# Optimization experiments

Measured on AMD Instinct MI355X. Metric: run time of the kernel, lower is better.

## Reference

```python
import jax, jax.numpy as jnp
import numpy as np
import math

M_FEAT = 8  # module-level m = 4 * 2


def theta(u, R):
    # Performer FAVOR random feature map: [cos(uR), sin(uR)] / sqrt(m)
    p = u @ R  # [b, t, m]
    return jnp.concatenate([jnp.cos(p), jnp.sin(p)], axis=-1) / math.sqrt(M_FEAT)


def setup_inputs() -> dict:
    key = jax.random.key(0)
    ks = jax.random.split(key, 8)
    n_embd, n_head = 1024, 16
    d_head = n_embd // n_head  # 64
    b, t = 4, 8192
    x = jax.random.normal(ks[0], (b, t, n_embd), dtype=jnp.float32)
    # random feature projection buffer w: [d_head, m]
    w = jax.random.normal(ks[1], (d_head, M_FEAT), dtype=jnp.float32)
    # nn.Linear(n_embd, d_head) weights (stored as [in, out] for x @ W) + biases
    s = 1.0 / math.sqrt(n_embd)
    Wq = jax.random.uniform(ks[2], (n_embd, d_head), minval=-s, maxval=s, dtype=jnp.float32)
    bq = jax.random.uniform(ks[3], (d_head,), minval=-s, maxval=s, dtype=jnp.float32)
    Wk = jax.random.uniform(ks[4], (n_embd, d_head), minval=-s, maxval=s, dtype=jnp.float32)
    bk = jax.random.uniform(ks[5], (d_head,), minval=-s, maxval=s, dtype=jnp.float32)
    Wv = jax.random.uniform(ks[6], (n_embd, d_head), minval=-s, maxval=s, dtype=jnp.float32)
    bv = jax.random.uniform(ks[7], (d_head,), minval=-s, maxval=s, dtype=jnp.float32)
    return {"x": x, "w": w, "Wq": Wq, "bq": bq, "Wk": Wk, "bk": bk, "Wv": Wv, "bv": bv}


def reference(x, w, Wq, bq, Wk, bk, Wv, bv):
    # Projections to per-head dim
    q = x @ Wq + bq  # [b, t, d_head]
    k = x @ Wk + bk
    v = x @ Wv + bv
    # FAVOR+ random feature maps (features concatenated on last dim)
    qP = theta(q, w)  # [b, t, 2m]
    Kp = theta(k, w)  # [b, t, 2m]
    # Linear attention: S = Kp^T @ V, then y = qP @ S  (O(t) instead of O(t^2))
    S = jnp.einsum('btm,btd->bmd', Kp, v)   # [b, 2m, d_head]
    y = jnp.einsum('btm,bmd->btd', qP, S)   # [b, t, d_head]
    return y
```

## Files before the change

kernel.cpp:

```cpp
#include <hip/hip_runtime.h>

#define E_DIM 1024
#define NROWS 32768
#define LDA 132
#define INV_SQRT8 0.35355339059327373f

typedef __bf16 bf16x8 __attribute__((ext_vector_type(8)));
typedef float f32x4 __attribute__((ext_vector_type(4)));

__global__ __launch_bounds__(256) void favor_setup(
    const float* __restrict__ w,
    const float* __restrict__ Wq,
    const float* __restrict__ bq,
    const float* __restrict__ Wk,
    const float* __restrict__ bk,
    const float* __restrict__ Wv,
    float* __restrict__ bqw,
    float* __restrict__ bkw,
    __bf16* __restrict__ WpHS,
    __bf16* __restrict__ WpLS,
    __bf16* __restrict__ WvS)
{
    const int g = blockIdx.x * 256 + threadIdx.x;
    {
        const int k = g >> 4;
        const int c = g & 15;
        const float* Wsrc = (c < 8) ? Wq : Wk;
        const int cc = c & 7;
        float s = 0.f;
        #pragma unroll 8
        for (int d = 0; d < 64; ++d)
            s += Wsrc[k * 64 + d] * w[d * 8 + cc];
        const __bf16 h = (__bf16)s;
        const int step = k >> 5, quad = (k >> 3) & 3, j = k & 7;
        const int lane = quad * 16 + c;
        const int idx = (step * 64 + lane) * 8 + j;
        WpHS[idx] = h;
        WpLS[idx] = (__bf16)(s - (float)h);
    }
    #pragma unroll
    for (int t = 0; t < 4; ++t) {
        const int idx = g * 4 + t;
        const int n = idx >> 10;
        const int k = idx & 1023;
        const int ct = n >> 4, l15 = n & 15;
        const int step = k >> 5, quad = (k >> 3) & 3, j = k & 7;
        const int lane = quad * 16 + l15;
        WvS[(((ct * 32 + step) * 64) + lane) * 8 + j] = (__bf16)Wv[k * 64 + n];
    }
    if (g < 16) {
        const int col = g & 7;
        const float* bb = (g < 8) ? bq : bk;
        float s1 = 0.f;
        #pragma unroll 8
        for (int d = 0; d < 64; ++d)
            s1 += bb[d] * w[d * 8 + col];
        if (g < 8) bqw[col] = s1; else bkw[col] = s1;
    }
}

__global__ __launch_bounds__(256, 4) void favor_main(
    const float* __restrict__ x,
    const __bf16* __restrict__ WvS,
    const __bf16* __restrict__ WpHS,
    const __bf16* __restrict__ WpLS,
    const float* __restrict__ bqw,
    const float* __restrict__ bkw,
    const float* __restrict__ bv,
    float* __restrict__ pq_out,
    float* __restrict__ Sbkt)
{
    __shared__ __align__(16) float smem[2 * 32 * LDA];
    float* tile0 = smem;
    float* tile1 = smem + 32 * LDA;
    float* bufA = smem;
    float* bufB = smem + 2816;
    float* bufC = smem + 5632;
    float* vb   = smem;
    float* kp   = smem + 2176;
    float* sred = smem + 2688;

    const int tid  = threadIdx.x;
    const int wg   = blockIdx.x;
    const int lane = tid & 63;
    const int wv   = __builtin_amdgcn_readfirstlane(tid >> 6);
    const int l15  = lane & 15;
    const int quad = lane >> 4;

    const int srow = tid >> 5;
    const int scol = (tid & 31) * 4;
    const float* xg = x + (long)(wg * 32 + srow) * E_DIM + scol;

    const int fra0 = l15 * LDA + wv * 32 + quad * 8;
    const int fra1 = fra0 + 16 * LDA;

    f32x4 zero = {0.f, 0.f, 0.f, 0.f};
    f32x4 accv[4][2];
    #pragma unroll
    for (int ct = 0; ct < 4; ++ct) { accv[ct][0] = zero; accv[ct][1] = zero; }
    f32x4 accp[2] = {zero, zero};

    float4 st[4];
    #pragma unroll
    for (int i = 0; i < 4; ++i) st[i] = *(const float4*)(xg + i * 8192);

    for (int s = 0; s < 8; ++s) {
        float* wb = (s & 1) ? tile1 : tile0;
        #pragma unroll
        for (int i = 0; i < 4; ++i)
            *(float4*)(wb + (srow + i * 8) * LDA + scol) = st[i];
        if (s < 7) {
            #pragma unroll
            for (int i = 0; i < 4; ++i)
                st[i] = *(const float4*)(xg + (s + 1) * 128 + i * 8192);
        }
        __syncthreads();

        bf16x8 ah0, al0, ah1, al1;
        {
            const float4 a0 = *(const float4*)(wb + fra0);
            const float4 a1 = *(const float4*)(wb + fra0 + 4);
            const float f[8] = {a0.x, a0.y, a0.z, a0.w, a1.x, a1.y, a1.z, a1.w};
            #pragma unroll
            for (int i = 0; i < 8; ++i) {
                const __bf16 h = (__bf16)f[i];
                ah0[i] = h; al0[i] = (__bf16)(f[i] - (float)h);
            }
        }
        {
            const float4 a0 = *(const float4*)(wb + fra1);
            const float4 a1 = *(const float4*)(wb + fra1 + 4);
            const float f[8] = {a0.x, a0.y, a0.z, a0.w, a1.x, a1.y, a1.z, a1.w};
            #pragma unroll
            for (int i = 0; i < 8; ++i) {
                const __bf16 h = (__bf16)f[i];
                ah1[i] = h; al1[i] = (__bf16)(f[i] - (float)h);
            }
        }
        const int gs = s * 4 + wv;
        const __bf16* bp = WvS + (long)gs * 512 + lane * 8;
        #pragma unroll
        for (int ct = 0; ct < 4; ++ct) {
            const bf16x8 b = *(const bf16x8*)(bp + ct * 16384);
            accv[ct][0] = __builtin_amdgcn_mfma_f32_16x16x32_bf16(ah0, b, accv[ct][0], 0, 0, 0);
            accv[ct][1] = __builtin_amdgcn_mfma_f32_16x16x32_bf16(ah1, b, accv[ct][1], 0, 0, 0);
        }
        {
            const bf16x8 bh = *(const bf16x8*)(WpHS + (long)gs * 512 + lane * 8);
            const bf16x8 bl = *(const bf16x8*)(WpLS + (long)gs * 512 + lane * 8);
            accp[0] = __builtin_amdgcn_mfma_f32_16x16x32_bf16(ah0, bh, accp[0], 0, 0, 0);
            accp[0] = __builtin_amdgcn_mfma_f32_16x16x32_bf16(al0, bh, accp[0], 0, 0, 0);
            accp[0] = __builtin_amdgcn_mfma_f32_16x16x32_bf16(ah0, bl, accp[0], 0, 0, 0);
            accp[1] = __builtin_amdgcn_mfma_f32_16x16x32_bf16(ah1, bh, accp[1], 0, 0, 0);
            accp[1] = __builtin_amdgcn_mfma_f32_16x16x32_bf16(al1, bh, accp[1], 0, 0, 0);
            accp[1] = __builtin_amdgcn_mfma_f32_16x16x32_bf16(ah1, bl, accp[1], 0, 0, 0);
        }
    }
    __syncthreads();

    if (wv == 1 || wv == 3) {
        float* dst = ((wv == 1) ? bufA : bufB) + lane * 44;
        #pragma unroll
        for (int ct = 0; ct < 4; ++ct) {
            *(f32x4*)(dst + (ct * 2 + 0) * 4) = accv[ct][0];
            *(f32x4*)(dst + (ct * 2 + 1) * 4) = accv[ct][1];
        }
        *(f32x4*)(dst + 32) = accp[0];
        *(f32x4*)(dst + 36) = accp[1];
    }
    __syncthreads();
    if (wv == 0 || wv == 2) {
        const float* src = ((wv == 0) ? bufA : bufB) + lane * 44;
        #pragma unroll
        for (int ct = 0; ct < 4; ++ct) {
            accv[ct][0] += *(const f32x4*)(src + (ct * 2 + 0) * 4);
            accv[ct][1] += *(const f32x4*)(src + (ct * 2 + 1) * 4);
        }
        accp[0] += *(const f32x4*)(src + 32);
        accp[1] += *(const f32x4*)(src + 36);
    }
    if (wv == 2) {
        float* dst = bufC + lane * 44;
        #pragma unroll
        for (int ct = 0; ct < 4; ++ct) {
            *(f32x4*)(dst + (ct * 2 + 0) * 4) = accv[ct][0];
            *(f32x4*)(dst + (ct * 2 + 1) * 4) = accv[ct][1];
        }
        *(f32x4*)(dst + 32) = accp[0];
        *(f32x4*)(dst + 36) = accp[1];
    }
    __syncthreads();
    if (wv == 0) {
        const float* src = bufC + lane * 44;
        #pragma unroll
        for (int ct = 0; ct < 4; ++ct) {
            accv[ct][0] += *(const f32x4*)(src + (ct * 2 + 0) * 4);
            accv[ct][1] += *(const f32x4*)(src + (ct * 2 + 1) * 4);
        }
        accp[0] += *(const f32x4*)(src + 32);
        accp[1] += *(const f32x4*)(src + 36);

        if (l15 < 8) {
            const float bq_ = bqw[l15];
            #pragma unroll
            for (int rh = 0; rh < 2; ++rh)
                #pragma unroll
                for (int r = 0; r < 4; ++r) {
                    const long gr = (long)wg * 32 + rh * 16 + quad * 4 + r;
                    pq_out[gr * 8 + l15] = accp[rh][r] + bq_;
                }
        } else {
            const float bk_ = bkw[l15 - 8];
            #pragma unroll
            for (int rh = 0; rh < 2; ++rh)
                #pragma unroll
                for (int r = 0; r < 4; ++r) {
                    const int lr = rh * 16 + quad * 4 + r;
                    const float pk_ = accp[rh][r] + bk_;
                    kp[lr * 16 + (l15 - 8)] = __cosf(pk_) * INV_SQRT8;
                    kp[lr * 16 + l15]       = __sinf(pk_) * INV_SQRT8;
                }
        }
        #pragma unroll
        for (int ct = 0; ct < 4; ++ct) {
            const float bv_ = bv[ct * 16 + l15];
            #pragma unroll
            for (int rh = 0; rh < 2; ++rh)
                #pragma unroll
                for (int r = 0; r < 4; ++r)
                    vb[(rh * 16 + quad * 4 + r) * 68 + ct * 16 + l15] = accv[ct][rh][r] + bv_;
        }
    }
    __syncthreads();

    {
        const int d4 = l15;
        const int mg = quad;
        const int rq = wv;
        float sa[16];
        #pragma unroll
        for (int i = 0; i < 16; ++i) sa[i] = 0.f;
        #pragma unroll
        for (int rr = 0; rr < 8; ++rr) {
            const int r = rq * 8 + rr;
            const float4 vv  = *(const float4*)(vb + r * 68 + d4 * 4);
            const float4 kk4 = *(const float4*)(kp + r * 16 + mg * 4);
            const float km[4] = {kk4.x, kk4.y, kk4.z, kk4.w};
            const float vm[4] = {vv.x, vv.y, vv.z, vv.w};
            #pragma unroll
            for (int mi = 0; mi < 4; ++mi)
                #pragma unroll
                for (int di = 0; di < 4; ++di)
                    sa[mi * 4 + di] += km[mi] * vm[di];
        }
        if (rq > 0) {
            float* dst = sred + (rq - 1) * 1280 + lane * 20;
            #pragma unroll
            for (int i = 0; i < 4; ++i)
                *(float4*)(dst + i * 4) = make_float4(sa[i*4], sa[i*4+1], sa[i*4+2], sa[i*4+3]);
        }
        __syncthreads();
        if (rq == 0) {
            #pragma unroll
            for (int j = 0; j < 3; ++j) {
                const float* src = sred + j * 1280 + lane * 20;
                #pragma unroll
                for (int i = 0; i < 16; ++i) sa[i] += src[i];
            }
            float* Sb = Sbkt + ((long)(wg & 31) * 4 + (wg >> 8)) * 1024;
            #pragma unroll
            for (int mi = 0; mi < 4; ++mi)
                #pragma unroll
                for (int di = 0; di < 4; ++di)
                    atomicAdd(&Sb[(mg * 4 + mi) * 64 + d4 * 4 + di], sa[mi * 4 + di]);
        }
    }
}

__global__ __launch_bounds__(256) void favor_reduce(
    const float* __restrict__ Sbkt,
    float* __restrict__ S)
{
    const int idx = blockIdx.x * 256 + threadIdx.x;
    float s = 0.f;
    #pragma unroll
    for (int j = 0; j < 32; ++j) s += Sbkt[j * 4096 + idx];
    S[idx] = s;
}

__global__ __launch_bounds__(256) void favor_out(
    const float* __restrict__ pq,
    const float* __restrict__ S,
    float* __restrict__ y)
{
    const int tid = threadIdx.x;
    const int blk = blockIdx.x;
    const int lane = tid & 63;
    const int w = __builtin_amdgcn_readfirstlane(tid >> 6);
    const long row = (long)blk * 64 + lane;
    const int b = blk >> 7;

    const float4 p0 = *(const float4*)(pq + row * 8);
    const float4 p1 = *(const float4*)(pq + row * 8 + 4);
    float qp[16];
    qp[0] = __cosf(p0.x) * INV_SQRT8;  qp[1] = __cosf(p0.y) * INV_SQRT8;
    qp[2] = __cosf(p0.z) * INV_SQRT8;  qp[3] = __cosf(p0.w) * INV_SQRT8;
    qp[4] = __cosf(p1.x) * INV_SQRT8;  qp[5] = __cosf(p1.y) * INV_SQRT8;
    qp[6] = __cosf(p1.z) * INV_SQRT8;  qp[7] = __cosf(p1.w) * INV_SQRT8;
    qp[8] = __sinf(p0.x) * INV_SQRT8;  qp[9] = __sinf(p0.y) * INV_SQRT8;
    qp[10]= __sinf(p0.z) * INV_SQRT8;  qp[11]= __sinf(p0.w) * INV_SQRT8;
    qp[12]= __sinf(p1.x) * INV_SQRT8;  qp[13]= __sinf(p1.y) * INV_SQRT8;
    qp[14]= __sinf(p1.z) * INV_SQRT8;  qp[15]= __sinf(p1.w) * INV_SQRT8;

    const float* Sb = S + b * 1024 + w * 16;
    float a[16];
    #pragma unroll
    for (int i = 0; i < 16; ++i) a[i] = 0.f;
    #pragma unroll
    for (int m = 0; m < 16; ++m) {
        const float4 s0 = *(const float4*)(Sb + m * 64);
        const float4 s1 = *(const float4*)(Sb + m * 64 + 4);
        const float4 s2 = *(const float4*)(Sb + m * 64 + 8);
        const float4 s3 = *(const float4*)(Sb + m * 64 + 12);
        const float qm = qp[m];
        a[0] += qm * s0.x;  a[1] += qm * s0.y;  a[2] += qm * s0.z;  a[3] += qm * s0.w;
        a[4] += qm * s1.x;  a[5] += qm * s1.y;  a[6] += qm * s1.z;  a[7] += qm * s1.w;
        a[8] += qm * s2.x;  a[9] += qm * s2.y;  a[10]+= qm * s2.z;  a[11]+= qm * s2.w;
        a[12]+= qm * s3.x;  a[13]+= qm * s3.y;  a[14]+= qm * s3.z;  a[15]+= qm * s3.w;
    }
    float* yp = y + row * 64 + w * 16;
    *(float4*)(yp)      = make_float4(a[0],  a[1],  a[2],  a[3]);
    *(float4*)(yp + 4)  = make_float4(a[4],  a[5],  a[6],  a[7]);
    *(float4*)(yp + 8)  = make_float4(a[8],  a[9],  a[10], a[11]);
    *(float4*)(yp + 12) = make_float4(a[12], a[13], a[14], a[15]);
}

extern "C" void kernel_launch(void* const* d_in, const int* in_sizes, int n_in,
                              void* d_out, int out_size, void* d_ws, size_t ws_size,
                              hipStream_t stream) {
    const float* x  = (const float*)d_in[0];
    const float* w  = (const float*)d_in[1];
    const float* Wq = (const float*)d_in[2];
    const float* bq = (const float*)d_in[3];
    const float* Wk = (const float*)d_in[4];
    const float* bk = (const float*)d_in[5];
    const float* Wv = (const float*)d_in[6];
    const float* bv = (const float*)d_in[7];
    float* y = (float*)d_out;

    char* ws = (char*)d_ws;
    float*  S    = (float*)(ws);
    float*  bqw  = (float*)(ws + 16384);
    float*  bkw  = (float*)(ws + 16448);
    __bf16* WpHS = (__bf16*)(ws + 32768);
    __bf16* WpLS = (__bf16*)(ws + 65536);
    __bf16* WvS  = (__bf16*)(ws + 98304);
    float*  Sbkt = (float*)(ws + 229376);
    float*  pq   = (float*)(ws + 786432);

    hipMemsetAsync(Sbkt, 0, 32 * 4096 * sizeof(float), stream);
    favor_setup<<<64, 256, 0, stream>>>(w, Wq, bq, Wk, bk, Wv, bqw, bkw, WpHS, WpLS, WvS);
    favor_main<<<1024, 256, 0, stream>>>(x, WvS, WpHS, WpLS, bqw, bkw, bv, pq, Sbkt);
    favor_reduce<<<16, 256, 0, stream>>>(Sbkt, S);
    favor_out<<<512, 256, 0, stream>>>(pq, S, y);
}
```

Baseline: 276.1 us.

## Stream x tiles directly into LDS with XOR swizzle and widen atomic buckets

Replaces the register-staged global-to-LDS copy of x with global_load_lds direct transfers into a double buffer. An XOR swizzle replaces the padded LDS layout to avoid bank conflicts, and the loop is fully unrolled with one barrier per stage. This is meant to cut VGPR pressure and the extra LDS store instructions in a kernel bound by x bandwidth. It also doubles the atomic accumulation buckets from 32 to 64 to reduce atomic contention, which adds work to the reduce kernel and to the memset.

```diff
diff --git a/kernel.cpp b/kernel.cpp
--- a/kernel.cpp
+++ b/kernel.cpp
@@ -1,12 +1,14 @@
 #include <hip/hip_runtime.h>
+#include <cstdint>
 
 #define E_DIM 1024
 #define NROWS 32768
-#define LDA 132
 #define INV_SQRT8 0.35355339059327373f
 
 typedef __bf16 bf16x8 __attribute__((ext_vector_type(8)));
 typedef float f32x4 __attribute__((ext_vector_type(4)));
+typedef const __attribute__((address_space(1))) void* gas_t;
+typedef __attribute__((address_space(3))) void* las_t;
 
 __global__ __launch_bounds__(256) void favor_setup(
     const float* __restrict__ w,
@@ -70,9 +72,9 @@
     float* __restrict__ pq_out,
     float* __restrict__ Sbkt)
 {
-    __shared__ __align__(16) float smem[2 * 32 * LDA];
+    __shared__ __align__(16) float smem[8448];
     float* tile0 = smem;
-    float* tile1 = smem + 32 * LDA;
+    float* tile1 = smem + 4096;
     float* bufA = smem;
     float* bufB = smem + 2816;
     float* bufC = smem + 5632;
@@ -87,12 +89,36 @@
     const int l15  = lane & 15;
     const int quad = lane >> 4;
 
-    const int srow = tid >> 5;
-    const int scol = (tid & 31) * 4;
-    const float* xg = x + (long)(wg * 32 + srow) * E_DIM + scol;
-
-    const int fra0 = l15 * LDA + wv * 32 + quad * 8;
-    const int fra1 = fra0 + 16 * LDA;
+    const int lrow_hi = lane >> 5;
+    const float *src0, *src1, *src2, *src3;
+    {
+        const long rowbase = (long)wg * 32;
+        const int r0 = wv * 8 + 0 + lrow_hi;
+        const int r1 = wv * 8 + 2 + lrow_hi;
+        const int r2 = wv * 8 + 4 + lrow_hi;
+        const int r3 = wv * 8 + 6 + lrow_hi;
+        src0 = x + (rowbase + r0) * E_DIM + (((lane & 31) ^ r0) * 4);
+        src1 = x + (rowbase + r1) * E_DIM + (((lane & 31) ^ r1) * 4);
+        src2 = x + (rowbase + r2) * E_DIM + (((lane & 31) ^ r2) * 4);
+        src3 = x + (rowbase + r3) * E_DIM + (((lane & 31) ^ r3) * 4);
+    }
+    const int lo0 = (wv * 8 + 0) * 128;
+    const int lo1 = (wv * 8 + 2) * 128;
+    const int lo2 = (wv * 8 + 4) * 128;
+    const int lo3 = (wv * 8 + 6) * 128;
+
+#define PF(tb, s)                                                                                        \
+    __builtin_amdgcn_global_load_lds((gas_t)(src0 + (s) * 128), (las_t)((tb) + lo0), 16, 0, 0);          \
+    __builtin_amdgcn_global_load_lds((gas_t)(src1 + (s) * 128), (las_t)((tb) + lo1), 16, 0, 0);          \
+    __builtin_amdgcn_global_load_lds((gas_t)(src2 + (s) * 128), (las_t)((tb) + lo2), 16, 0, 0);          \
+    __builtin_amdgcn_global_load_lds((gas_t)(src3 + (s) * 128), (las_t)((tb) + lo3), 16, 0, 0);
+
+    const int u0 = wv * 8 + quad * 2;
+    const int fr0 = l15, fr1 = l15 + 16;
+    const int fa00 = (fr0 * 128 + ((u0 ^ fr0) * 4)) * 4;
+    const int fa01 = (fr0 * 128 + (((u0 + 1) ^ fr0) * 4)) * 4;
+    const int fa10 = (fr1 * 128 + ((u0 ^ fr1) * 4)) * 4;
+    const int fa11 = (fr1 * 128 + (((u0 + 1) ^ fr1) * 4)) * 4;
 
     f32x4 zero = {0.f, 0.f, 0.f, 0.f};
     f32x4 accv[4][2];
@@ -100,26 +126,20 @@
     for (int ct = 0; ct < 4; ++ct) { accv[ct][0] = zero; accv[ct][1] = zero; }
     f32x4 accp[2] = {zero, zero};
 
-    float4 st[4];
-    #pragma unroll
-    for (int i = 0; i < 4; ++i) st[i] = *(const float4*)(xg + i * 8192);
-
+    PF(tile0, 0)
+    __syncthreads();
+
+    #pragma unroll
     for (int s = 0; s < 8; ++s) {
         float* wb = (s & 1) ? tile1 : tile0;
-        #pragma unroll
-        for (int i = 0; i < 4; ++i)
-            *(float4*)(wb + (srow + i * 8) * LDA + scol) = st[i];
         if (s < 7) {
-            #pragma unroll
-            for (int i = 0; i < 4; ++i)
-                st[i] = *(const float4*)(xg + (s + 1) * 128 + i * 8192);
-        }
-        __syncthreads();
-
+            float* nb = (s & 1) ? tile0 : tile1;
+            PF(nb, s + 1)
+        }
         bf16x8 ah0, al0, ah1, al1;
         {
-            const float4 a0 = *(const float4*)(wb + fra0);
-            const float4 a1 = *(const float4*)(wb + fra0 + 4);
+            const float4 a0 = *(const float4*)((const char*)wb + fa00);
+            const float4 a1 = *(const float4*)((const char*)wb + fa01);
             const float f[8] = {a0.x, a0.y, a0.z, a0.w, a1.x, a1.y, a1.z, a1.w};
             #pragma unroll
             for (int i = 0; i < 8; ++i) {
@@ -128,8 +148,8 @@
             }
         }
         {
-            const float4 a0 = *(const float4*)(wb + fra1);
-            const float4 a1 = *(const float4*)(wb + fra1 + 4);
+            const float4 a0 = *(const float4*)((const char*)wb + fa10);
+            const float4 a1 = *(const float4*)((const char*)wb + fa11);
             const float f[8] = {a0.x, a0.y, a0.z, a0.w, a1.x, a1.y, a1.z, a1.w};
             #pragma unroll
             for (int i = 0; i < 8; ++i) {
@@ -155,8 +175,9 @@
             accp[1] = __builtin_amdgcn_mfma_f32_16x16x32_bf16(al1, bh, accp[1], 0, 0, 0);
             accp[1] = __builtin_amdgcn_mfma_f32_16x16x32_bf16(ah1, bl, accp[1], 0, 0, 0);
         }
-    }
-    __syncthreads();
+        __syncthreads();
+    }
+#undef PF
 
     if (wv == 1 || wv == 3) {
         float* dst = ((wv == 1) ? bufA : bufB) + lane * 44;
@@ -267,7 +288,7 @@
                 #pragma unroll
                 for (int i = 0; i < 16; ++i) sa[i] += src[i];
             }
-            float* Sb = Sbkt + ((long)(wg & 31) * 4 + (wg >> 8)) * 1024;
+            float* Sb = Sbkt + ((long)(wg & 63) * 4 + (wg >> 8)) * 1024;
             #pragma unroll
             for (int mi = 0; mi < 4; ++mi)
                 #pragma unroll
@@ -281,11 +302,13 @@
     const float* __restrict__ Sbkt,
     float* __restrict__ S)
 {
-    const int idx = blockIdx.x * 256 + threadIdx.x;
+    const int b   = blockIdx.x >> 2;
+    const int col = (blockIdx.x & 3) * 256 + threadIdx.x;
     float s = 0.f;
-    #pragma unroll
-    for (int j = 0; j < 32; ++j) s += Sbkt[j * 4096 + idx];
-    S[idx] = s;
+    #pragma unroll 8
+    for (int j = 0; j < 64; ++j)
+        s += Sbkt[((long)j * 4 + b) * 1024 + col];
+    S[b * 1024 + col] = s;
 }
 
 __global__ __launch_bounds__(256) void favor_out(
@@ -356,9 +379,9 @@
     __bf16* WpLS = (__bf16*)(ws + 65536);
     __bf16* WvS  = (__bf16*)(ws + 98304);
     float*  Sbkt = (float*)(ws + 229376);
-    float*  pq   = (float*)(ws + 786432);
-
-    hipMemsetAsync(Sbkt, 0, 32 * 4096 * sizeof(float), stream);
+    float*  pq   = (float*)(ws + 1277952);
+
+    hipMemsetAsync(Sbkt, 0, 64 * 4 * 1024 * sizeof(float), stream);
     favor_setup<<<64, 256, 0, stream>>>(w, Wq, bq, Wk, bk, Wv, bqw, bkw, WpHS, WpLS, WvS);
     favor_main<<<1024, 256, 0, stream>>>(x, WvS, WpHS, WpLS, bqw, bkw, bv, pq, Sbkt);
     favor_reduce<<<16, 256, 0, stream>>>(Sbkt, S);
```

Measured after the change: 239.1 us. 13.4% less time.

## Load full 16-row x tile via direct global-to-LDS loads and split K across waves

Applied to the files above, without the earlier changes.

The main kernel now handles 16 rows per block (2048 blocks) and loads the whole 16x1024 x tile in one shot with global_load_lds, instead of register-staged double buffering over 32 rows. Each wave takes a quarter of the K dimension, and partial sums are reduced through LDS. The bucketed S partial buffer grows to 128 buckets with a matching reduce kernel. The output kernel stages y through shared memory so global stores are fully coalesced. The aim is less register staging overhead and more memory-level parallelism, at the cost of lower occupancy (launch bounds 2), more LDS per block, and a larger reduction buffer.

```diff
diff --git a/kernel.cpp b/kernel.cpp
--- a/kernel.cpp
+++ b/kernel.cpp
@@ -1,12 +1,15 @@
 #include <hip/hip_runtime.h>
+#include <cstdint>
 
 #define E_DIM 1024
 #define NROWS 32768
-#define LDA 132
+#define LDT 1028
 #define INV_SQRT8 0.35355339059327373f
 
 typedef __bf16 bf16x8 __attribute__((ext_vector_type(8)));
 typedef float f32x4 __attribute__((ext_vector_type(4)));
+typedef const __attribute__((address_space(1))) void* gas_t;
+typedef __attribute__((address_space(3))) void* las_t;
 
 __global__ __launch_bounds__(256) void favor_setup(
     const float* __restrict__ w,
@@ -59,7 +62,7 @@
     }
 }
 
-__global__ __launch_bounds__(256, 4) void favor_main(
+__global__ __launch_bounds__(256, 2) void favor_main(
     const float* __restrict__ x,
     const __bf16* __restrict__ WvS,
     const __bf16* __restrict__ WpHS,
@@ -70,15 +73,11 @@
     float* __restrict__ pq_out,
     float* __restrict__ Sbkt)
 {
-    __shared__ __align__(16) float smem[2 * 32 * LDA];
-    float* tile0 = smem;
-    float* tile1 = smem + 32 * LDA;
-    float* bufA = smem;
-    float* bufB = smem + 2816;
-    float* bufC = smem + 5632;
-    float* vb   = smem;
-    float* kp   = smem + 2176;
-    float* sred = smem + 2688;
+    __shared__ __align__(16) float smem[16 * LDT];
+    float* bufW = smem;
+    float* vb   = smem + 4096;
+    float* kp   = smem + 5248;
+    float* sred = smem + 5632;
 
     const int tid  = threadIdx.x;
     const int wg   = blockIdx.x;
@@ -87,148 +86,98 @@
     const int l15  = lane & 15;
     const int quad = lane >> 4;
 
-    const int srow = tid >> 5;
-    const int scol = (tid & 31) * 4;
-    const float* xg = x + (long)(wg * 32 + srow) * E_DIM + scol;
-
-    const int fra0 = l15 * LDA + wv * 32 + quad * 8;
-    const int fra1 = fra0 + 16 * LDA;
+    {
+        const int sr = wv * 4;
+        const float* xs = x + ((long)wg * 16 + sr) * E_DIM + lane * 4;
+        #pragma unroll
+        for (int r = 0; r < 4; ++r)
+            #pragma unroll
+            for (int c = 0; c < 4; ++c)
+                __builtin_amdgcn_global_load_lds(
+                    (gas_t)(xs + r * E_DIM + c * 256),
+                    (las_t)(smem + (sr + r) * LDT + c * 256), 16, 0, 0);
+    }
 
     f32x4 zero = {0.f, 0.f, 0.f, 0.f};
-    f32x4 accv[4][2];
-    #pragma unroll
-    for (int ct = 0; ct < 4; ++ct) { accv[ct][0] = zero; accv[ct][1] = zero; }
-    f32x4 accp[2] = {zero, zero};
-
-    float4 st[4];
-    #pragma unroll
-    for (int i = 0; i < 4; ++i) st[i] = *(const float4*)(xg + i * 8192);
-
-    for (int s = 0; s < 8; ++s) {
-        float* wb = (s & 1) ? tile1 : tile0;
-        #pragma unroll
-        for (int i = 0; i < 4; ++i)
-            *(float4*)(wb + (srow + i * 8) * LDA + scol) = st[i];
-        if (s < 7) {
-            #pragma unroll
-            for (int i = 0; i < 4; ++i)
-                st[i] = *(const float4*)(xg + (s + 1) * 128 + i * 8192);
-        }
-        __syncthreads();
-
-        bf16x8 ah0, al0, ah1, al1;
+    f32x4 accv[4];
+    #pragma unroll
+    for (int ct = 0; ct < 4; ++ct) accv[ct] = zero;
+    f32x4 accp = zero;
+
+    __syncthreads();
+
+    const int cb = wv * 256;
+    #pragma unroll
+    for (int ks = 0; ks < 8; ++ks) {
+        const float* ap = smem + l15 * LDT + cb + ks * 32 + quad * 8;
+        const float4 a0 = *(const float4*)ap;
+        const float4 a1 = *(const float4*)(ap + 4);
+        bf16x8 ah, al;
         {
-            const float4 a0 = *(const float4*)(wb + fra0);
-            const float4 a1 = *(const float4*)(wb + fra0 + 4);
             const float f[8] = {a0.x, a0.y, a0.z, a0.w, a1.x, a1.y, a1.z, a1.w};
             #pragma unroll
             for (int i = 0; i < 8; ++i) {
                 const __bf16 h = (__bf16)f[i];
-                ah0[i] = h; al0[i] = (__bf16)(f[i] - (float)h);
+                ah[i] = h; al[i] = (__bf16)(f[i] - (float)h);
             }
         }
-        {
-            const float4 a0 = *(const float4*)(wb + fra1);
-            const float4 a1 = *(const float4*)(wb + fra1 + 4);
-            const float f[8] = {a0.x, a0.y, a0.z, a0.w, a1.x, a1.y, a1.z, a1.w};
-            #pragma unroll
-            for (int i = 0; i < 8; ++i) {
-                const __bf16 h = (__bf16)f[i];
-                ah1[i] = h; al1[i] = (__bf16)(f[i] - (float)h);
-            }
-        }
-        const int gs = s * 4 + wv;
+        const int gs = wv * 8 + ks;
         const __bf16* bp = WvS + (long)gs * 512 + lane * 8;
         #pragma unroll
         for (int ct = 0; ct < 4; ++ct) {
             const bf16x8 b = *(const bf16x8*)(bp + ct * 16384);
-            accv[ct][0] = __builtin_amdgcn_mfma_f32_16x16x32_bf16(ah0, b, accv[ct][0], 0, 0, 0);
-            accv[ct][1] = __builtin_amdgcn_mfma_f32_16x16x32_bf16(ah1, b, accv[ct][1], 0, 0, 0);
+            accv[ct] = __builtin_amdgcn_mfma_f32_16x16x32_bf16(ah, b, accv[ct], 0, 0, 0);
         }
         {
             const bf16x8 bh = *(const bf16x8*)(WpHS + (long)gs * 512 + lane * 8);
             const bf16x8 bl = *(const bf16x8*)(WpLS + (long)gs * 512 + lane * 8);
-            accp[0] = __builtin_amdgcn_mfma_f32_16x16x32_bf16(ah0, bh, accp[0], 0, 0, 0);
-            accp[0] = __builtin_amdgcn_mfma_f32_16x16x32_bf16(al0, bh, accp[0], 0, 0, 0);
-            accp[0] = __builtin_amdgcn_mfma_f32_16x16x32_bf16(ah0, bl, accp[0], 0, 0, 0);
-            accp[1] = __builtin_amdgcn_mfma_f32_16x16x32_bf16(ah1, bh, accp[1], 0, 0, 0);
-            accp[1] = __builtin_amdgcn_mfma_f32_16x16x32_bf16(al1, bh, accp[1], 0, 0, 0);
-            accp[1] = __builtin_amdgcn_mfma_f32_16x16x32_bf16(ah1, bl, accp[1], 0, 0, 0);
-        }
-    }
-    __syncthreads();
-
-    if (wv == 1 || wv == 3) {
-        float* dst = ((wv == 1) ? bufA : bufB) + lane * 44;
-        #pragma unroll
-        for (int ct = 0; ct < 4; ++ct) {
-            *(f32x4*)(dst + (ct * 2 + 0) * 4) = accv[ct][0];
-            *(f32x4*)(dst + (ct * 2 + 1) * 4) = accv[ct][1];
-        }
-        *(f32x4*)(dst + 32) = accp[0];
-        *(f32x4*)(dst + 36) = accp[1];
-    }
-    __syncthreads();
-    if (wv == 0 || wv == 2) {
-        const float* src = ((wv == 0) ? bufA : bufB) + lane * 44;
-        #pragma unroll
-        for (int ct = 0; ct < 4; ++ct) {
-            accv[ct][0] += *(const f32x4*)(src + (ct * 2 + 0) * 4);
-            accv[ct][1] += *(const f32x4*)(src + (ct * 2 + 1) * 4);
-        }
-        accp[0] += *(const f32x4*)(src + 32);
-        accp[1] += *(const f32x4*)(src + 36);
-    }
-    if (wv == 2) {
-        float* dst = bufC + lane * 44;
-        #pragma unroll
-        for (int ct = 0; ct < 4; ++ct) {
-            *(f32x4*)(dst + (ct * 2 + 0) * 4) = accv[ct][0];
-            *(f32x4*)(dst + (ct * 2 + 1) * 4) = accv[ct][1];
-        }
-        *(f32x4*)(dst + 32) = accp[0];
-        *(f32x4*)(dst + 36) = accp[1];
+            accp = __builtin_amdgcn_mfma_f32_16x16x32_bf16(ah, bh, accp, 0, 0, 0);
+            accp = __builtin_amdgcn_mfma_f32_16x16x32_bf16(al, bh, accp, 0, 0, 0);
+            accp = __builtin_amdgcn_mfma_f32_16x16x32_bf16(ah, bl, accp, 0, 0, 0);
+        }
+    }
+    __syncthreads();
+
+    if (wv != 0) {
+        float* dst = bufW + ((wv - 1) * 64 + lane) * 20;
+        #pragma unroll
+        for (int ct = 0; ct < 4; ++ct)
+            *(f32x4*)(dst + ct * 4) = accv[ct];
+        *(f32x4*)(dst + 16) = accp;
     }
     __syncthreads();
     if (wv == 0) {
-        const float* src = bufC + lane * 44;
-        #pragma unroll
-        for (int ct = 0; ct < 4; ++ct) {
-            accv[ct][0] += *(const f32x4*)(src + (ct * 2 + 0) * 4);
-            accv[ct][1] += *(const f32x4*)(src + (ct * 2 + 1) * 4);
-        }
-        accp[0] += *(const f32x4*)(src + 32);
-        accp[1] += *(const f32x4*)(src + 36);
-
+        #pragma unroll
+        for (int j = 0; j < 3; ++j) {
+            const float* src = bufW + (j * 64 + lane) * 20;
+            #pragma unroll
+            for (int ct = 0; ct < 4; ++ct)
+                accv[ct] += *(const f32x4*)(src + ct * 4);
+            accp += *(const f32x4*)(src + 16);
+        }
         if (l15 < 8) {
             const float bq_ = bqw[l15];
             #pragma unroll
-            for (int rh = 0; rh < 2; ++rh)
-                #pragma unroll
-                for (int r = 0; r < 4; ++r) {
-                    const long gr = (long)wg * 32 + rh * 16 + quad * 4 + r;
-                    pq_out[gr * 8 + l15] = accp[rh][r] + bq_;
-                }
+            for (int r = 0; r < 4; ++r) {
+                const long gr = (long)wg * 16 + quad * 4 + r;
+                pq_out[gr * 8 + l15] = accp[r] + bq_;
+            }
         } else {
             const float bk_ = bkw[l15 - 8];
             #pragma unroll
-            for (int rh = 0; rh < 2; ++rh)
-                #pragma unroll
-                for (int r = 0; r < 4; ++r) {
-                    const int lr = rh * 16 + quad * 4 + r;
-                    const float pk_ = accp[rh][r] + bk_;
-                    kp[lr * 16 + (l15 - 8)] = __cosf(pk_) * INV_SQRT8;
-                    kp[lr * 16 + l15]       = __sinf(pk_) * INV_SQRT8;
-                }
+            for (int r = 0; r < 4; ++r) {
+                const int lr = quad * 4 + r;
+                const float pk_ = accp[r] + bk_;
+                kp[lr * 16 + (l15 - 8)] = __cosf(pk_) * INV_SQRT8;
+                kp[lr * 16 + l15]       = __sinf(pk_) * INV_SQRT8;
+            }
         }
         #pragma unroll
         for (int ct = 0; ct < 4; ++ct) {
             const float bv_ = bv[ct * 16 + l15];
             #pragma unroll
-            for (int rh = 0; rh < 2; ++rh)
-                #pragma unroll
-                for (int r = 0; r < 4; ++r)
-                    vb[(rh * 16 + quad * 4 + r) * 68 + ct * 16 + l15] = accv[ct][rh][r] + bv_;
+            for (int r = 0; r < 4; ++r)
+                vb[(quad * 4 + r) * 68 + ct * 16 + l15] = accv[ct][r] + bv_;
         }
     }
     __syncthreads();
@@ -241,8 +190,8 @@
         #pragma unroll
         for (int i = 0; i < 16; ++i) sa[i] = 0.f;
         #pragma unroll
-        for (int rr = 0; rr < 8; ++rr) {
-            const int r = rq * 8 + rr;
+        for (int rr = 0; rr < 4; ++rr) {
+            const int r = rq * 4 + rr;
             const float4 vv  = *(const float4*)(vb + r * 68 + d4 * 4);
             const float4 kk4 = *(const float4*)(kp + r * 16 + mg * 4);
             const float km[4] = {kk4.x, kk4.y, kk4.z, kk4.w};
@@ -254,7 +203,7 @@
                     sa[mi * 4 + di] += km[mi] * vm[di];
         }
         if (rq > 0) {
-            float* dst = sred + (rq - 1) * 1280 + lane * 20;
+            float* dst = sred + ((rq - 1) * 64 + lane) * 20;
             #pragma unroll
             for (int i = 0; i < 4; ++i)
                 *(float4*)(dst + i * 4) = make_float4(sa[i*4], sa[i*4+1], sa[i*4+2], sa[i*4+3]);
@@ -263,11 +212,11 @@
         if (rq == 0) {
             #pragma unroll
             for (int j = 0; j < 3; ++j) {
-                const float* src = sred + j * 1280 + lane * 20;
+                const float* src = sred + (j * 64 + lane) * 20;
                 #pragma unroll
                 for (int i = 0; i < 16; ++i) sa[i] += src[i];
             }
-            float* Sb = Sbkt + ((long)(wg & 31) * 4 + (wg >> 8)) * 1024;
+            float* Sb = Sbkt + ((long)(wg & 127) * 4 + (wg >> 9)) * 1024;
             #pragma unroll
             for (int mi = 0; mi < 4; ++mi)
                 #pragma unroll
@@ -281,11 +230,14 @@
     const float* __restrict__ Sbkt,
     float* __restrict__ S)
 {
-    const int idx = blockIdx.x * 256 + threadIdx.x;
+    const int g = blockIdx.x * 256 + threadIdx.x;
+    const int b = g >> 10;
+    const int col = g & 1023;
     float s = 0.f;
-    #pragma unroll
-    for (int j = 0; j < 32; ++j) s += Sbkt[j * 4096 + idx];
-    S[idx] = s;
+    #pragma unroll 8
+    for (int j = 0; j < 128; ++j)
+        s += Sbkt[((long)j * 4 + b) * 1024 + col];
+    S[b * 1024 + col] = s;
 }
 
 __global__ __launch_bounds__(256) void favor_out(
@@ -293,6 +245,8 @@
     const float* __restrict__ S,
     float* __restrict__ y)
 {
+    __shared__ __align__(16) float Ly[64 * 68];
+
     const int tid = threadIdx.x;
     const int blk = blockIdx.x;
     const int lane = tid & 63;
@@ -328,11 +282,23 @@
         a[8] += qm * s2.x;  a[9] += qm * s2.y;  a[10]+= qm * s2.z;  a[11]+= qm * s2.w;
         a[12]+= qm * s3.x;  a[13]+= qm * s3.y;  a[14]+= qm * s3.z;  a[15]+= qm * s3.w;
     }
-    float* yp = y + row * 64 + w * 16;
-    *(float4*)(yp)      = make_float4(a[0],  a[1],  a[2],  a[3]);
-    *(float4*)(yp + 4)  = make_float4(a[4],  a[5],  a[6],  a[7]);
-    *(float4*)(yp + 8)  = make_float4(a[8],  a[9],  a[10], a[11]);
-    *(float4*)(yp + 12) = make_float4(a[12], a[13], a[14], a[15]);
+    {
+        float* lw = Ly + lane * 68 + w * 16;
+        *(float4*)(lw)      = make_float4(a[0],  a[1],  a[2],  a[3]);
+        *(float4*)(lw + 4)  = make_float4(a[4],  a[5],  a[6],  a[7]);
+        *(float4*)(lw + 8)  = make_float4(a[8],  a[9],  a[10], a[11]);
+        *(float4*)(lw + 12) = make_float4(a[12], a[13], a[14], a[15]);
+    }
+    __syncthreads();
+    {
+        const float* ls = Ly + (w * 16 + (lane >> 4)) * 68 + (lane & 15) * 4;
+        float* yb = y + (long)blk * 4096 + w * 1024 + lane * 4;
+        #pragma unroll
+        for (int i = 0; i < 4; ++i) {
+            const float4 v = *(const float4*)(ls + i * 4 * 68);
+            *(float4*)(yb + i * 256) = v;
+        }
+    }
 }
 
 extern "C" void kernel_launch(void* const* d_in, const int* in_sizes, int n_in,
@@ -356,11 +322,11 @@
     __bf16* WpLS = (__bf16*)(ws + 65536);
     __bf16* WvS  = (__bf16*)(ws + 98304);
     float*  Sbkt = (float*)(ws + 229376);
-    float*  pq   = (float*)(ws + 786432);
-
-    hipMemsetAsync(Sbkt, 0, 32 * 4096 * sizeof(float), stream);
+    float*  pq   = (float*)(ws + 2326528);
+
+    hipMemsetAsync(Sbkt, 0, 128 * 4 * 1024 * sizeof(float), stream);
     favor_setup<<<64, 256, 0, stream>>>(w, Wq, bq, Wk, bk, Wv, bqw, bkw, WpHS, WpLS, WvS);
-    favor_main<<<1024, 256, 0, stream>>>(x, WvS, WpHS, WpLS, bqw, bkw, bv, pq, Sbkt);
+    favor_main<<<2048, 256, 0, stream>>>(x, WvS, WpHS, WpLS, bqw, bkw, bv, pq, Sbkt);
     favor_reduce<<<16, 256, 0, stream>>>(Sbkt, S);
     favor_out<<<512, 256, 0, stream>>>(pq, S, y);
 }
```

Result: faster. 260.6 us (-5.6%).
